# Performance work log

Measured on AMD Instinct MI355X. Metric: run time of the kernel, lower is better.

Reference implementation:

```python
import jax, jax.numpy as jnp
import numpy as np
from jax.scipy.special import logsumexp

TEMPERATURE = 0.1
EPS = 1e-8  # matches torch F.cosine_similarity eps


def setup_inputs() -> dict:
    key = jax.random.key(0)
    k1, k2 = jax.random.split(key)
    N, D, NUM_CLASSES = 8192, 256, 64
    embeddings = jax.random.normal(k1, (N, D), dtype=jnp.float32)
    target = jax.random.randint(k2, (N,), 0, NUM_CLASSES, dtype=jnp.int64)
    return {"embeddings": embeddings, "target": target}


def reference(embeddings, target):
    N = target.shape[0]
    # cosine similarity: normalize rows, then a single GEMM for all pairs
    norms = jnp.linalg.norm(embeddings, axis=-1, keepdims=True)
    e = embeddings / jnp.maximum(norms, EPS)
    sim = (e @ e.T) / TEMPERATURE  # [N, N]

    pos = target[:, None] == target[None, :]  # [N, N] bool, incl. diagonal
    diag = jnp.eye(N, dtype=bool)
    neg_inf = jnp.asarray(-jnp.inf, dtype=sim.dtype)

    # denominator: negatives only (positives masked to -inf)
    lse_neg = logsumexp(jnp.where(pos, neg_inf, sim), axis=1)
    # numerator: positives excluding self (diagonal masked to -inf)
    lse_pos = logsumexp(jnp.where(pos & ~diag, sim, neg_inf), axis=1)

    loss = lse_neg - lse_pos
    return loss.sum()
```

## Files before the change

kernel.cpp:

```cpp
#include <hip/hip_runtime.h>
#include <hip/hip_bf16.h>
#include <stdint.h>
#include <math.h>

#define NROWS 8192
#define DIM   256
#define RB    256
#define BI    128
#define JSUB  64
#define NBJS  8
#define JBLK  (JSUB*NBJS)
#define NG    (NROWS/JBLK)
#define NIT   (NROWS/BI)
#define NCLS  64
#define CAP   256

typedef __attribute__((ext_vector_type(4)))  int   int4v;
typedef __attribute__((ext_vector_type(8)))  int   int8v;
typedef __attribute__((ext_vector_type(16))) float floatx16;

typedef const __attribute__((address_space(1))) uint32_t gas_u32;
typedef __attribute__((address_space(3))) uint32_t las_u32;

#define SCALE_1_16 0x7B7B7B7B
#define L2E10      14.4269504088896f
#define CA_SCALE   (L2E10 * 16.0f)
#define CB_SCALE   16.0f

#if __has_builtin(__builtin_amdgcn_exp2f)
#define EXP2(x) __builtin_amdgcn_exp2f(x)
#else
#define EXP2(x) exp2f(x)
#endif

__device__ __forceinline__ void gload_lds16(const void* g, void* l) {
    __builtin_amdgcn_global_load_lds((gas_u32*)(uintptr_t)g,
                                     (las_u32*)(uintptr_t)l, 16, 0, 0);
}

__global__ __launch_bounds__(256) void normalize_kernel(const float* __restrict__ emb,
                                                        uint32_t* __restrict__ a8,
                                                        uint32_t* __restrict__ b8,
                                                        float* __restrict__ out)
{
    if (blockIdx.x == 0 && threadIdx.x == 0) *out = 0.f;
    int row  = blockIdx.x * 4 + (threadIdx.x >> 6);
    int lane = threadIdx.x & 63;
    float4 v = ((const float4*)(emb + (size_t)row * DIM))[lane];
    float ss = v.x*v.x + v.y*v.y + v.z*v.z + v.w*v.w;
    #pragma unroll
    for (int off = 32; off > 0; off >>= 1)
        ss += __shfl_xor(ss, off, 64);
    float inv = 1.0f / fmaxf(sqrtf(ss), 1e-8f);
    float ia = CA_SCALE * inv, ib = CB_SCALE * inv;
    int ra = __builtin_amdgcn_cvt_pk_fp8_f32(v.x * ia, v.y * ia, 0, false);
    ra     = __builtin_amdgcn_cvt_pk_fp8_f32(v.z * ia, v.w * ia, ra, true);
    int rb = __builtin_amdgcn_cvt_pk_fp8_f32(v.x * ib, v.y * ib, 0, false);
    rb     = __builtin_amdgcn_cvt_pk_fp8_f32(v.z * ib, v.w * ib, rb, true);
    a8[(size_t)row * 64 + lane] = (uint32_t)ra;
    b8[(size_t)row * 64 + lane] = (uint32_t)rb;
}

template<bool DIAG>
__device__ __forceinline__ void epi(const floatx16 acc[2],
                                    int jbs, int h, int ic0, float& ts)
{
    #pragma unroll
    for (int jt = 0; jt < 2; ++jt)
        #pragma unroll
        for (int rq = 0; rq < 4; ++rq)
            #pragma unroll
            for (int r2 = 0; r2 < 4; ++r2) {
                float v = EXP2(acc[jt][rq * 4 + r2]);
                if (DIAG) {
                    const int jg_ = jbs + jt * 32 + rq * 8 + h * 4 + r2;
                    if (jg_ == ic0) v = 0.f;
                }
                ts += v;
            }
}

__global__ __launch_bounds__(256, 4) void fused_kernel(const uint8_t* __restrict__ eA,
                                                       const uint8_t* __restrict__ eB,
                                                       const int* __restrict__ tgt,
                                                       float* __restrict__ pts,
                                                       float* __restrict__ sp)
{
    __shared__ uint8_t smem[2 * JSUB * RB];

    const int tid  = threadIdx.x;
    const int wave = tid >> 6;
    const int lane = tid & 63;
    const int col  = lane & 31;
    const int h    = lane >> 5;

    if (blockIdx.x < NCLS) {
        int* idx = (int*)smem;
        int* cnt = (int*)(smem + CAP * 4);
        const int c = blockIdx.x;
        if (tid == 0) *cnt = 0;
        __syncthreads();
        int4v tv[8];
        #pragma unroll
        for (int k = 0; k < 8; ++k)
            tv[k] = *(const int4v*)(tgt + k * 1024 + tid * 4);
        #pragma unroll
        for (int k = 0; k < 8; ++k)
            #pragma unroll
            for (int r = 0; r < 4; ++r)
                if (tv[k][r] == c) {
                    int p = atomicAdd(cnt, 1);
                    if (p < CAP) idx[p] = k * 1024 + tid * 4 + r;
                }
        __syncthreads();
        const int M   = min(*cnt, CAP);
        const int Mp  = (M + 31) & ~31;
        const int nbt = Mp >> 5;

        for (int bt = wave; bt < nbt; bt += 4) {
            const int b = bt * 32 + col;
            const uint8_t* pb = eB + (size_t)idx[min(b, M - 1)] * RB + h * 32;
            int8v bfr[4];
            #pragma unroll
            for (int s = 0; s < 4; ++s)
                bfr[s] = *(const int8v*)(pb + s * 64);
            float psum = 0.f;
            for (int at = 0; at < nbt; ++at) {
                const uint8_t* pa = eA + (size_t)idx[min(at * 32 + col, M - 1)] * RB + h * 32;
                floatx16 acc = (floatx16){0.f,0.f,0.f,0.f,0.f,0.f,0.f,0.f,
                                          0.f,0.f,0.f,0.f,0.f,0.f,0.f,0.f};
                #pragma unroll
                for (int s = 0; s < 4; ++s) {
                    int8v af = *(const int8v*)(pa + s * 64);
                    acc = __builtin_amdgcn_mfma_scale_f32_32x32x64_f8f6f4(
                        af, bfr[s], acc, 0, 0, 0, SCALE_1_16, 0, SCALE_1_16);
                }
                #pragma unroll
                for (int rq = 0; rq < 4; ++rq)
                    #pragma unroll
                    for (int r2 = 0; r2 < 4; ++r2) {
                        const int a = at * 32 + rq * 8 + h * 4 + r2;
                        float v = EXP2(acc[rq * 4 + r2]);
                        psum += (a != b && a < M) ? v : 0.f;
                    }
            }
            psum += __shfl_xor(psum, 32, 64);
            if (h == 0 && b < M) sp[idx[b]] = psum;
        }
        return;
    }

    const int g  = blockIdx.x - NCLS;
    const int bi = g & (NIT - 1);
    const int jg = g >> 6;

    const uint8_t* pb = eB + (size_t)(bi * BI + wave * 32 + col) * RB + h * 32;
    int8v bfr[4];
    #pragma unroll
    for (int s = 0; s < 4; ++s)
        bfr[s] = *(const int8v*)(pb + s * 64);

    int goffA[4];
    #pragma unroll
    for (int t = 0; t < 4; ++t) {
        int s   = wave * 256 + t * 64 + lane;
        int row = s >> 4;
        int lc  = (s & 15) ^ (row & 15);
        goffA[t] = row * RB + lc * 16;
    }
    const char* gA = (const char*)(eA + (size_t)jg * JBLK * RB);

    #pragma unroll
    for (int t = 0; t < 4; ++t)
        gload_lds16(gA + goffA[t], smem + wave * 4096 + t * 1024);

    const int ic0 = bi * BI + wave * 32 + col;

    const int xm = col & 15;
    int poff[4];
    #pragma unroll
    for (int s = 0; s < 4; ++s)
        poff[s] = ((s * 4 + h * 2) ^ xm) << 4;

    __syncthreads();

    float ts = 0.f;
    const int dpair = bi - jg * 4;

    #pragma unroll
    for (int bjs = 0; bjs < NBJS; ++bjs) {
        if (bjs < NBJS - 1) {
            const char* gAn = gA + (size_t)(bjs + 1) * JSUB * RB;
            #pragma unroll
            for (int t = 0; t < 4; ++t)
                gload_lds16(gAn + goffA[t],
                            smem + ((bjs + 1) & 1) * (JSUB * RB) + wave * 4096 + t * 1024);
        }

        const uint8_t* ab = smem + (bjs & 1) * (JSUB * RB);
        floatx16 acc[2];
        #pragma unroll
        for (int jt = 0; jt < 2; ++jt)
            acc[jt] = (floatx16){0.f,0.f,0.f,0.f,0.f,0.f,0.f,0.f,
                                 0.f,0.f,0.f,0.f,0.f,0.f,0.f,0.f};

        #pragma unroll
        for (int s = 0; s < 4; ++s) {
            int8v af[2];
            #pragma unroll
            for (int jt = 0; jt < 2; ++jt) {
                const uint8_t* pa = ab + (size_t)(jt * 32 + col) * RB;
                int4v lo = *(const int4v*)(pa + poff[s]);
                int4v hi = *(const int4v*)(pa + (poff[s] ^ 16));
                af[jt] = __builtin_shufflevector(lo, hi, 0, 1, 2, 3, 4, 5, 6, 7);
            }
            #pragma unroll
            for (int jt = 0; jt < 2; ++jt)
                acc[jt] = __builtin_amdgcn_mfma_scale_f32_32x32x64_f8f6f4(
                    af[jt], bfr[s], acc[jt], 0, 0,
                    0, SCALE_1_16, 0, SCALE_1_16);
        }

        const int jbs = jg * JBLK + bjs * JSUB;
        if ((bjs >> 1) == dpair)
            epi<true >(acc, jbs, h, ic0, ts);
        else
            epi<false>(acc, jbs, h, ic0, ts);

        if (bjs < NBJS - 1)
            __syncthreads();
    }

    ts += __shfl_xor(ts, 32, 64);
    if (h == 0)
        pts[(size_t)jg * NROWS + ic0] = ts;
}

__global__ __launch_bounds__(256) void finalize_kernel(const float* __restrict__ pts,
                                                       const float* __restrict__ sp,
                                                       float* __restrict__ out)
{
    const int i = blockIdx.x * 256 + threadIdx.x;
    float st = 0.f;
    #pragma unroll
    for (int t = 0; t < NG; ++t)
        st += pts[(size_t)t * NROWS + i];
    const float spv = sp[i];
    const float ns  = st - spv;
    float loss = logf(ns) - logf(spv);
    #pragma unroll
    for (int off = 32; off > 0; off >>= 1)
        loss += __shfl_xor(loss, off, 64);
    __shared__ float w4[4];
    if ((threadIdx.x & 63) == 0) w4[threadIdx.x >> 6] = loss;
    __syncthreads();
    if (threadIdx.x == 0)
        atomicAdd(out, w4[0] + w4[1] + w4[2] + w4[3]);
}

extern "C" void kernel_launch(void* const* d_in, const int* in_sizes, int n_in,
                              void* d_out, int out_size, void* d_ws, size_t ws_size,
                              hipStream_t stream)
{
    (void)in_sizes; (void)n_in; (void)out_size; (void)ws_size;
    const float* emb = (const float*)d_in[0];
    const int*   tgt = (const int*)d_in[1];
    float*       out = (float*)d_out;

    uint32_t* a8  = (uint32_t*)d_ws;
    uint32_t* b8  = a8 + (size_t)NROWS * 64;
    float*    pts = (float*)(b8 + (size_t)NROWS * 64);
    float*    sp  = pts + (size_t)NG * NROWS;

    normalize_kernel<<<NROWS / 4, 256, 0, stream>>>(emb, a8, b8, out);

    fused_kernel<<<NCLS + NIT * NG, 256, 0, stream>>>(
        (const uint8_t*)a8, (const uint8_t*)b8, tgt, pts, sp);

    finalize_kernel<<<NROWS / 256, 256, 0, stream>>>(pts, sp, out);
}
```

Measured before the change: 83.40 us.

## Double per-wave B-row tile so each LDS A fragment feeds four MFMAs

Doubles the row block from 128 to 256, so each wave now keeps B fragments for 64 rows in registers and issues four MFMAs per A fragment read from shared memory instead of two. This halves the number of grid blocks and the number of times each A tile is staged through LDS, which cuts global and LDS traffic per FLOP. In exchange, register use roughly doubles, launch bounds drop to 2 blocks per SM, and occupancy and latency hiding fall. The diagonal-masking block index and output indexing are adjusted to match.

```diff
diff --git a/kernel.cpp b/kernel.cpp
--- a/kernel.cpp
+++ b/kernel.cpp
@@ -6,7 +6,7 @@
 #define NROWS 8192
 #define DIM   256
 #define RB    256
-#define BI    128
+#define BI    256
 #define JSUB  64
 #define NBJS  8
 #define JBLK  (JSUB*NBJS)
@@ -62,25 +62,22 @@
 }
 
 template<bool DIAG>
-__device__ __forceinline__ void epi(const floatx16 acc[2],
-                                    int jbs, int h, int ic0, float& ts)
-{
-    #pragma unroll
-    for (int jt = 0; jt < 2; ++jt)
-        #pragma unroll
-        for (int rq = 0; rq < 4; ++rq)
-            #pragma unroll
-            for (int r2 = 0; r2 < 4; ++r2) {
-                float v = EXP2(acc[jt][rq * 4 + r2]);
-                if (DIAG) {
-                    const int jg_ = jbs + jt * 32 + rq * 8 + h * 4 + r2;
-                    if (jg_ == ic0) v = 0.f;
-                }
-                ts += v;
+__device__ __forceinline__ void epi1(const floatx16& a, int jbase, int h, int ic, float& ts)
+{
+    #pragma unroll
+    for (int rq = 0; rq < 4; ++rq)
+        #pragma unroll
+        for (int r2 = 0; r2 < 4; ++r2) {
+            float v = EXP2(a[rq * 4 + r2]);
+            if (DIAG) {
+                const int jg_ = jbase + rq * 8 + h * 4 + r2;
+                if (jg_ == ic) v = 0.f;
             }
-}
-
-__global__ __launch_bounds__(256, 4) void fused_kernel(const uint8_t* __restrict__ eA,
+            ts += v;
+        }
+}
+
+__global__ __launch_bounds__(256, 2) void fused_kernel(const uint8_t* __restrict__ eA,
                                                        const uint8_t* __restrict__ eB,
                                                        const int* __restrict__ tgt,
                                                        float* __restrict__ pts,
@@ -152,13 +149,17 @@
 
     const int g  = blockIdx.x - NCLS;
     const int bi = g & (NIT - 1);
-    const int jg = g >> 6;
-
-    const uint8_t* pb = eB + (size_t)(bi * BI + wave * 32 + col) * RB + h * 32;
-    int8v bfr[4];
-    #pragma unroll
-    for (int s = 0; s < 4; ++s)
-        bfr[s] = *(const int8v*)(pb + s * 64);
+    const int jg = g >> 5;
+
+    const uint8_t* pb0 = eB + (size_t)(bi * BI + wave * 64 + col) * RB + h * 32;
+    int8v bfr[2][4];
+    #pragma unroll
+    for (int ib = 0; ib < 2; ++ib) {
+        const uint8_t* pb = pb0 + (size_t)(ib * 32) * RB;
+        #pragma unroll
+        for (int s = 0; s < 4; ++s)
+            bfr[ib][s] = *(const int8v*)(pb + s * 64);
+    }
 
     int goffA[4];
     #pragma unroll
@@ -174,7 +175,7 @@
     for (int t = 0; t < 4; ++t)
         gload_lds16(gA + goffA[t], smem + wave * 4096 + t * 1024);
 
-    const int ic0 = bi * BI + wave * 32 + col;
+    const int ic0 = bi * BI + wave * 64 + col;
 
     const int xm = col & 15;
     int poff[4];
@@ -184,8 +185,8 @@
 
     __syncthreads();
 
-    float ts = 0.f;
-    const int dpair = bi - jg * 4;
+    float ts[2] = {0.f, 0.f};
+    const int dquad = bi - 2 * jg;
 
     #pragma unroll
     for (int bjs = 0; bjs < NBJS; ++bjs) {
@@ -198,11 +199,13 @@
         }
 
         const uint8_t* ab = smem + (bjs & 1) * (JSUB * RB);
-        floatx16 acc[2];
-        #pragma unroll
-        for (int jt = 0; jt < 2; ++jt)
-            acc[jt] = (floatx16){0.f,0.f,0.f,0.f,0.f,0.f,0.f,0.f,
-                                 0.f,0.f,0.f,0.f,0.f,0.f,0.f,0.f};
+        floatx16 acc[2][2];
+        #pragma unroll
+        for (int ib = 0; ib < 2; ++ib)
+            #pragma unroll
+            for (int jt = 0; jt < 2; ++jt)
+                acc[ib][jt] = (floatx16){0.f,0.f,0.f,0.f,0.f,0.f,0.f,0.f,
+                                         0.f,0.f,0.f,0.f,0.f,0.f,0.f,0.f};
 
         #pragma unroll
         for (int s = 0; s < 4; ++s) {
@@ -215,25 +218,39 @@
                 af[jt] = __builtin_shufflevector(lo, hi, 0, 1, 2, 3, 4, 5, 6, 7);
             }
             #pragma unroll
-            for (int jt = 0; jt < 2; ++jt)
-                acc[jt] = __builtin_amdgcn_mfma_scale_f32_32x32x64_f8f6f4(
-                    af[jt], bfr[s], acc[jt], 0, 0,
-                    0, SCALE_1_16, 0, SCALE_1_16);
+            for (int ib = 0; ib < 2; ++ib)
+                #pragma unroll
+                for (int jt = 0; jt < 2; ++jt)
+                    acc[ib][jt] = __builtin_amdgcn_mfma_scale_f32_32x32x64_f8f6f4(
+                        af[jt], bfr[ib][s], acc[ib][jt], 0, 0,
+                        0, SCALE_1_16, 0, SCALE_1_16);
         }
 
         const int jbs = jg * JBLK + bjs * JSUB;
-        if ((bjs >> 1) == dpair)
-            epi<true >(acc, jbs, h, ic0, ts);
-        else
-            epi<false>(acc, jbs, h, ic0, ts);
+        if ((bjs >> 2) == dquad) {
+            #pragma unroll
+            for (int ib = 0; ib < 2; ++ib)
+                #pragma unroll
+                for (int jt = 0; jt < 2; ++jt)
+                    epi1<true >(acc[ib][jt], jbs + jt * 32, h, ic0 + ib * 32, ts[ib]);
+        } else {
+            #pragma unroll
+            for (int ib = 0; ib < 2; ++ib)
+                #pragma unroll
+                for (int jt = 0; jt < 2; ++jt)
+                    epi1<false>(acc[ib][jt], jbs + jt * 32, h, ic0 + ib * 32, ts[ib]);
+        }
 
         if (bjs < NBJS - 1)
             __syncthreads();
     }
 
-    ts += __shfl_xor(ts, 32, 64);
-    if (h == 0)
-        pts[(size_t)jg * NROWS + ic0] = ts;
+    #pragma unroll
+    for (int ib = 0; ib < 2; ++ib) {
+        ts[ib] += __shfl_xor(ts[ib], 32, 64);
+        if (h == 0)
+            pts[(size_t)jg * NROWS + ic0 + ib * 32] = ts[ib];
+    }
 }
 
 __global__ __launch_bounds__(256) void finalize_kernel(const float* __restrict__ pts,
```

Result: slower. 87.53 us (+5.0%).

## Fuse finalize reduction into fused kernel via atomic ticket last-blocks

Applied to the files above, without the earlier changes.

Removes the separate finalize kernel launch. Each block of the fused kernel takes an atomic ticket when it finishes, and the last 32 blocks spin until every block has finished, then do the per-row log and sum reduction. This saves one launch and its gap, at the cost of a global counter, memory fences and spin-waiting in the tail blocks. Ticket order guarantees the waiting blocks are the last ones, so the spin-wait should not deadlock.

```diff
diff --git a/kernel.cpp b/kernel.cpp
--- a/kernel.cpp
+++ b/kernel.cpp
@@ -14,6 +14,8 @@
 #define NIT   (NROWS/BI)
 #define NCLS  64
 #define CAP   256
+#define TBLK  (NCLS + NIT*NG)
+#define NFIN  32
 
 typedef __attribute__((ext_vector_type(4)))  int   int4v;
 typedef __attribute__((ext_vector_type(8)))  int   int8v;
@@ -41,9 +43,10 @@
 __global__ __launch_bounds__(256) void normalize_kernel(const float* __restrict__ emb,
                                                         uint32_t* __restrict__ a8,
                                                         uint32_t* __restrict__ b8,
-                                                        float* __restrict__ out)
-{
-    if (blockIdx.x == 0 && threadIdx.x == 0) *out = 0.f;
+                                                        float* __restrict__ out,
+                                                        int* __restrict__ cc)
+{
+    if (blockIdx.x == 0 && threadIdx.x == 0) { *out = 0.f; *cc = 0; }
     int row  = blockIdx.x * 4 + (threadIdx.x >> 6);
     int lane = threadIdx.x & 63;
     float4 v = ((const float4*)(emb + (size_t)row * DIM))[lane];
@@ -84,9 +87,13 @@
                                                        const uint8_t* __restrict__ eB,
                                                        const int* __restrict__ tgt,
                                                        float* __restrict__ pts,
-                                                       float* __restrict__ sp)
+                                                       float* __restrict__ sp,
+                                                       int* __restrict__ cc,
+                                                       float* __restrict__ out)
 {
     __shared__ uint8_t smem[2 * JSUB * RB];
+    __shared__ int   ticket_s;
+    __shared__ float w4[4];
 
     const int tid  = threadIdx.x;
     const int wave = tid >> 6;
@@ -147,100 +154,106 @@
             psum += __shfl_xor(psum, 32, 64);
             if (h == 0 && b < M) sp[idx[b]] = psum;
         }
-        return;
+    } else {
+        const int g  = blockIdx.x - NCLS;
+        const int bi = g & (NIT - 1);
+        const int jg = g >> 6;
+
+        const uint8_t* pb = eB + (size_t)(bi * BI + wave * 32 + col) * RB + h * 32;
+        int8v bfr[4];
+        #pragma unroll
+        for (int s = 0; s < 4; ++s)
+            bfr[s] = *(const int8v*)(pb + s * 64);
+
+        int goffA[4];
+        #pragma unroll
+        for (int t = 0; t < 4; ++t) {
+            int s   = wave * 256 + t * 64 + lane;
+            int row = s >> 4;
+            int lc  = (s & 15) ^ (row & 15);
+            goffA[t] = row * RB + lc * 16;
+        }
+        const char* gA = (const char*)(eA + (size_t)jg * JBLK * RB);
+
+        #pragma unroll
+        for (int t = 0; t < 4; ++t)
+            gload_lds16(gA + goffA[t], smem + wave * 4096 + t * 1024);
+
+        const int ic0 = bi * BI + wave * 32 + col;
+
+        const int xm = col & 15;
+        int poff[4];
+        #pragma unroll
+        for (int s = 0; s < 4; ++s)
+            poff[s] = ((s * 4 + h * 2) ^ xm) << 4;
+
+        __syncthreads();
+
+        float ts = 0.f;
+        const int dpair = bi - jg * 4;
+
+        #pragma unroll
+        for (int bjs = 0; bjs < NBJS; ++bjs) {
+            if (bjs < NBJS - 1) {
+                const char* gAn = gA + (size_t)(bjs + 1) * JSUB * RB;
+                #pragma unroll
+                for (int t = 0; t < 4; ++t)
+                    gload_lds16(gAn + goffA[t],
+                                smem + ((bjs + 1) & 1) * (JSUB * RB) + wave * 4096 + t * 1024);
+            }
+
+            const uint8_t* ab = smem + (bjs & 1) * (JSUB * RB);
+            floatx16 acc[2];
+            #pragma unroll
+            for (int jt = 0; jt < 2; ++jt)
+                acc[jt] = (floatx16){0.f,0.f,0.f,0.f,0.f,0.f,0.f,0.f,
+                                     0.f,0.f,0.f,0.f,0.f,0.f,0.f,0.f};
+
+            #pragma unroll
+            for (int s = 0; s < 4; ++s) {
+                int8v af[2];
+                #pragma unroll
+                for (int jt = 0; jt < 2; ++jt) {
+                    const uint8_t* pa = ab + (size_t)(jt * 32 + col) * RB;
+                    int4v lo = *(const int4v*)(pa + poff[s]);
+                    int4v hi = *(const int4v*)(pa + (poff[s] ^ 16));
+                    af[jt] = __builtin_shufflevector(lo, hi, 0, 1, 2, 3, 4, 5, 6, 7);
+                }
+                #pragma unroll
+                for (int jt = 0; jt < 2; ++jt)
+                    acc[jt] = __builtin_amdgcn_mfma_scale_f32_32x32x64_f8f6f4(
+                        af[jt], bfr[s], acc[jt], 0, 0,
+                        0, SCALE_1_16, 0, SCALE_1_16);
+            }
+
+            const int jbs = jg * JBLK + bjs * JSUB;
+            if ((bjs >> 1) == dpair)
+                epi<true >(acc, jbs, h, ic0, ts);
+            else
+                epi<false>(acc, jbs, h, ic0, ts);
+
+            if (bjs < NBJS - 1)
+                __syncthreads();
+        }
+
+        ts += __shfl_xor(ts, 32, 64);
+        if (h == 0)
+            pts[(size_t)jg * NROWS + ic0] = ts;
     }
 
-    const int g  = blockIdx.x - NCLS;
-    const int bi = g & (NIT - 1);
-    const int jg = g >> 6;
-
-    const uint8_t* pb = eB + (size_t)(bi * BI + wave * 32 + col) * RB + h * 32;
-    int8v bfr[4];
-    #pragma unroll
-    for (int s = 0; s < 4; ++s)
-        bfr[s] = *(const int8v*)(pb + s * 64);
-
-    int goffA[4];
-    #pragma unroll
-    for (int t = 0; t < 4; ++t) {
-        int s   = wave * 256 + t * 64 + lane;
-        int row = s >> 4;
-        int lc  = (s & 15) ^ (row & 15);
-        goffA[t] = row * RB + lc * 16;
-    }
-    const char* gA = (const char*)(eA + (size_t)jg * JBLK * RB);
-
-    #pragma unroll
-    for (int t = 0; t < 4; ++t)
-        gload_lds16(gA + goffA[t], smem + wave * 4096 + t * 1024);
-
-    const int ic0 = bi * BI + wave * 32 + col;
-
-    const int xm = col & 15;
-    int poff[4];
-    #pragma unroll
-    for (int s = 0; s < 4; ++s)
-        poff[s] = ((s * 4 + h * 2) ^ xm) << 4;
-
-    __syncthreads();
-
-    float ts = 0.f;
-    const int dpair = bi - jg * 4;
-
-    #pragma unroll
-    for (int bjs = 0; bjs < NBJS; ++bjs) {
-        if (bjs < NBJS - 1) {
-            const char* gAn = gA + (size_t)(bjs + 1) * JSUB * RB;
-            #pragma unroll
-            for (int t = 0; t < 4; ++t)
-                gload_lds16(gAn + goffA[t],
-                            smem + ((bjs + 1) & 1) * (JSUB * RB) + wave * 4096 + t * 1024);
-        }
-
-        const uint8_t* ab = smem + (bjs & 1) * (JSUB * RB);
-        floatx16 acc[2];
-        #pragma unroll
-        for (int jt = 0; jt < 2; ++jt)
-            acc[jt] = (floatx16){0.f,0.f,0.f,0.f,0.f,0.f,0.f,0.f,
-                                 0.f,0.f,0.f,0.f,0.f,0.f,0.f,0.f};
-
-        #pragma unroll
-        for (int s = 0; s < 4; ++s) {
-            int8v af[2];
-            #pragma unroll
-            for (int jt = 0; jt < 2; ++jt) {
-                const uint8_t* pa = ab + (size_t)(jt * 32 + col) * RB;
-                int4v lo = *(const int4v*)(pa + poff[s]);
-                int4v hi = *(const int4v*)(pa + (poff[s] ^ 16));
-                af[jt] = __builtin_shufflevector(lo, hi, 0, 1, 2, 3, 4, 5, 6, 7);
-            }
-            #pragma unroll
-            for (int jt = 0; jt < 2; ++jt)
-                acc[jt] = __builtin_amdgcn_mfma_scale_f32_32x32x64_f8f6f4(
-                    af[jt], bfr[s], acc[jt], 0, 0,
-                    0, SCALE_1_16, 0, SCALE_1_16);
-        }
-
-        const int jbs = jg * JBLK + bjs * JSUB;
-        if ((bjs >> 1) == dpair)
-            epi<true >(acc, jbs, h, ic0, ts);
-        else
-            epi<false>(acc, jbs, h, ic0, ts);
-
-        if (bjs < NBJS - 1)
-            __syncthreads();
-    }
-
-    ts += __shfl_xor(ts, 32, 64);
-    if (h == 0)
-        pts[(size_t)jg * NROWS + ic0] = ts;
-}
-
-__global__ __launch_bounds__(256) void finalize_kernel(const float* __restrict__ pts,
-                                                       const float* __restrict__ sp,
-                                                       float* __restrict__ out)
-{
-    const int i = blockIdx.x * 256 + threadIdx.x;
+    __threadfence();
+    __syncthreads();
+    if (tid == 0) ticket_s = atomicAdd(cc, 1);
+    __syncthreads();
+    const int ticket = ticket_s;
+    if (ticket < TBLK - NFIN) return;
+
+    if (tid == 0)
+        while (atomicAdd(cc, 0) < TBLK) {}
+    __syncthreads();
+    __threadfence();
+
+    const int i = (ticket - (TBLK - NFIN)) * 256 + tid;
     float st = 0.f;
     #pragma unroll
     for (int t = 0; t < NG; ++t)
@@ -251,10 +264,9 @@
     #pragma unroll
     for (int off = 32; off > 0; off >>= 1)
         loss += __shfl_xor(loss, off, 64);
-    __shared__ float w4[4];
-    if ((threadIdx.x & 63) == 0) w4[threadIdx.x >> 6] = loss;
-    __syncthreads();
-    if (threadIdx.x == 0)
+    if (lane == 0) w4[wave] = loss;
+    __syncthreads();
+    if (tid == 0)
         atomicAdd(out, w4[0] + w4[1] + w4[2] + w4[3]);
 }
 
@@ -271,11 +283,10 @@
     uint32_t* b8  = a8 + (size_t)NROWS * 64;
     float*    pts = (float*)(b8 + (size_t)NROWS * 64);
     float*    sp  = pts + (size_t)NG * NROWS;
-
-    normalize_kernel<<<NROWS / 4, 256, 0, stream>>>(emb, a8, b8, out);
-
-    fused_kernel<<<NCLS + NIT * NG, 256, 0, stream>>>(
-        (const uint8_t*)a8, (const uint8_t*)b8, tgt, pts, sp);
-
-    finalize_kernel<<<NROWS / 256, 256, 0, stream>>>(pts, sp, out);
-}
+    int*      cc  = (int*)(sp + NROWS);
+
+    normalize_kernel<<<NROWS / 4, 256, 0, stream>>>(emb, a8, b8, out, cc);
+
+    fused_kernel<<<TBLK, 256, 0, stream>>>(
+        (const uint8_t*)a8, (const uint8_t*)b8, tgt, pts, sp, cc, out);
+}
```

New measurement: 169.2 us. 2.03x slower.

## Store single fp8 matrix in MFMA-fragment layout and load operands directly from global

Applied to the files above, without the earlier changes.

Replaces the two separately scaled fp8 copies (A scaled by log2e/T·16, B by 16) with one copy scaled by sqrt of the product, so the Gram-matrix scale is split symmetrically. The copy is written in a tiled layout where each 32-row block's MFMA fragments are contiguous. The fused kernel then reads A fragments straight from global/L2 with 32-byte vector loads, dropping the LDS double-buffer, the swizzled async global-to-LDS copies and the per-step barriers. This halves the normalize output and removes sync overhead. The cost is that every wave refetches A tiles from cache with no LDS reuse, and the symmetric scaling changes fp8 quantisation error.

```diff
diff --git a/kernel.cpp b/kernel.cpp
--- a/kernel.cpp
+++ b/kernel.cpp
@@ -5,7 +5,6 @@
 
 #define NROWS 8192
 #define DIM   256
-#define RB    256
 #define BI    128
 #define JSUB  64
 #define NBJS  8
@@ -19,13 +18,9 @@
 typedef __attribute__((ext_vector_type(8)))  int   int8v;
 typedef __attribute__((ext_vector_type(16))) float floatx16;
 
-typedef const __attribute__((address_space(1))) uint32_t gas_u32;
-typedef __attribute__((address_space(3))) uint32_t las_u32;
-
 #define SCALE_1_16 0x7B7B7B7B
 #define L2E10      14.4269504088896f
-#define CA_SCALE   (L2E10 * 16.0f)
-#define CB_SCALE   16.0f
+#define CE         60.772499831f
 
 #if __has_builtin(__builtin_amdgcn_exp2f)
 #define EXP2(x) __builtin_amdgcn_exp2f(x)
@@ -33,14 +28,9 @@
 #define EXP2(x) exp2f(x)
 #endif
 
-__device__ __forceinline__ void gload_lds16(const void* g, void* l) {
-    __builtin_amdgcn_global_load_lds((gas_u32*)(uintptr_t)g,
-                                     (las_u32*)(uintptr_t)l, 16, 0, 0);
-}
 
 __global__ __launch_bounds__(256) void normalize_kernel(const float* __restrict__ emb,
-                                                        uint32_t* __restrict__ a8,
-                                                        uint32_t* __restrict__ b8,
+                                                        uint32_t* __restrict__ e8,
                                                         float* __restrict__ out)
 {
     if (blockIdx.x == 0 && threadIdx.x == 0) *out = 0.f;
@@ -51,14 +41,11 @@
     #pragma unroll
     for (int off = 32; off > 0; off >>= 1)
         ss += __shfl_xor(ss, off, 64);
-    float inv = 1.0f / fmaxf(sqrtf(ss), 1e-8f);
-    float ia = CA_SCALE * inv, ib = CB_SCALE * inv;
-    int ra = __builtin_amdgcn_cvt_pk_fp8_f32(v.x * ia, v.y * ia, 0, false);
-    ra     = __builtin_amdgcn_cvt_pk_fp8_f32(v.z * ia, v.w * ia, ra, true);
-    int rb = __builtin_amdgcn_cvt_pk_fp8_f32(v.x * ib, v.y * ib, 0, false);
-    rb     = __builtin_amdgcn_cvt_pk_fp8_f32(v.z * ib, v.w * ib, rb, true);
-    a8[(size_t)row * 64 + lane] = (uint32_t)ra;
-    b8[(size_t)row * 64 + lane] = (uint32_t)rb;
+    float inv = CE / fmaxf(sqrtf(ss), 1e-8f);
+    int rw = __builtin_amdgcn_cvt_pk_fp8_f32(v.x * inv, v.y * inv, 0, false);
+    rw     = __builtin_amdgcn_cvt_pk_fp8_f32(v.z * inv, v.w * inv, rw, true);
+    e8[((size_t)(row >> 5) * 8 + (lane >> 3)) * 256 + (row & 31) * 8 + (lane & 7)] =
+        (uint32_t)rw;
 }
 
 template<bool DIAG>
@@ -80,13 +67,13 @@
             }
 }
 
-__global__ __launch_bounds__(256, 4) void fused_kernel(const uint8_t* __restrict__ eA,
-                                                       const uint8_t* __restrict__ eB,
+__global__ __launch_bounds__(256, 4) void fused_kernel(const uint8_t* __restrict__ E,
                                                        const int* __restrict__ tgt,
                                                        float* __restrict__ pts,
                                                        float* __restrict__ sp)
 {
-    __shared__ uint8_t smem[2 * JSUB * RB];
+    __shared__ int idx[CAP];
+    __shared__ int cnt;
 
     const int tid  = threadIdx.x;
     const int wave = tid >> 6;
@@ -95,10 +82,8 @@
     const int h    = lane >> 5;
 
     if (blockIdx.x < NCLS) {
-        int* idx = (int*)smem;
-        int* cnt = (int*)(smem + CAP * 4);
         const int c = blockIdx.x;
-        if (tid == 0) *cnt = 0;
+        if (tid == 0) cnt = 0;
         __syncthreads();
         int4v tv[8];
         #pragma unroll
@@ -109,29 +94,31 @@
             #pragma unroll
             for (int r = 0; r < 4; ++r)
                 if (tv[k][r] == c) {
-                    int p = atomicAdd(cnt, 1);
+                    int p = atomicAdd(&cnt, 1);
                     if (p < CAP) idx[p] = k * 1024 + tid * 4 + r;
                 }
         __syncthreads();
-        const int M   = min(*cnt, CAP);
+        const int M   = min(cnt, CAP);
         const int Mp  = (M + 31) & ~31;
         const int nbt = Mp >> 5;
 
         for (int bt = wave; bt < nbt; bt += 4) {
-            const int b = bt * 32 + col;
-            const uint8_t* pb = eB + (size_t)idx[min(b, M - 1)] * RB + h * 32;
+            const int b  = bt * 32 + col;
+            const int rb = idx[min(b, M - 1)];
+            const uint8_t* pb = E + (size_t)(rb >> 5) * 8192 + (rb & 31) * 32 + h * 1024;
             int8v bfr[4];
             #pragma unroll
             for (int s = 0; s < 4; ++s)
-                bfr[s] = *(const int8v*)(pb + s * 64);
+                bfr[s] = *(const int8v*)(pb + s * 2048);
             float psum = 0.f;
             for (int at = 0; at < nbt; ++at) {
-                const uint8_t* pa = eA + (size_t)idx[min(at * 32 + col, M - 1)] * RB + h * 32;
+                const int ra = idx[min(at * 32 + col, M - 1)];
+                const uint8_t* pa = E + (size_t)(ra >> 5) * 8192 + (ra & 31) * 32 + h * 1024;
                 floatx16 acc = (floatx16){0.f,0.f,0.f,0.f,0.f,0.f,0.f,0.f,
                                           0.f,0.f,0.f,0.f,0.f,0.f,0.f,0.f};
                 #pragma unroll
                 for (int s = 0; s < 4; ++s) {
-                    int8v af = *(const int8v*)(pa + s * 64);
+                    int8v af = *(const int8v*)(pa + s * 2048);
                     acc = __builtin_amdgcn_mfma_scale_f32_32x32x64_f8f6f4(
                         af, bfr[s], acc, 0, 0, 0, SCALE_1_16, 0, SCALE_1_16);
                 }
@@ -154,50 +141,22 @@
     const int bi = g & (NIT - 1);
     const int jg = g >> 6;
 
-    const uint8_t* pb = eB + (size_t)(bi * BI + wave * 32 + col) * RB + h * 32;
+    const uint8_t* pB = E + (size_t)(bi * 4 + wave) * 8192 + col * 32 + h * 1024;
     int8v bfr[4];
     #pragma unroll
     for (int s = 0; s < 4; ++s)
-        bfr[s] = *(const int8v*)(pb + s * 64);
-
-    int goffA[4];
-    #pragma unroll
-    for (int t = 0; t < 4; ++t) {
-        int s   = wave * 256 + t * 64 + lane;
-        int row = s >> 4;
-        int lc  = (s & 15) ^ (row & 15);
-        goffA[t] = row * RB + lc * 16;
-    }
-    const char* gA = (const char*)(eA + (size_t)jg * JBLK * RB);
-
-    #pragma unroll
-    for (int t = 0; t < 4; ++t)
-        gload_lds16(gA + goffA[t], smem + wave * 4096 + t * 1024);
+        bfr[s] = *(const int8v*)(pB + s * 2048);
 
     const int ic0 = bi * BI + wave * 32 + col;
-
-    const int xm = col & 15;
-    int poff[4];
-    #pragma unroll
-    for (int s = 0; s < 4; ++s)
-        poff[s] = ((s * 4 + h * 2) ^ xm) << 4;
-
-    __syncthreads();
+    const uint8_t* pA0 = E + (size_t)(jg * 16) * 8192 + col * 32 + h * 1024;
 
     float ts = 0.f;
     const int dpair = bi - jg * 4;
 
     #pragma unroll
     for (int bjs = 0; bjs < NBJS; ++bjs) {
-        if (bjs < NBJS - 1) {
-            const char* gAn = gA + (size_t)(bjs + 1) * JSUB * RB;
-            #pragma unroll
-            for (int t = 0; t < 4; ++t)
-                gload_lds16(gAn + goffA[t],
-                            smem + ((bjs + 1) & 1) * (JSUB * RB) + wave * 4096 + t * 1024);
-        }
-
-        const uint8_t* ab = smem + (bjs & 1) * (JSUB * RB);
+        const uint8_t* pA = pA0 + (size_t)bjs * 16384;
+
         floatx16 acc[2];
         #pragma unroll
         for (int jt = 0; jt < 2; ++jt)
@@ -206,19 +165,13 @@
 
         #pragma unroll
         for (int s = 0; s < 4; ++s) {
-            int8v af[2];
             #pragma unroll
             for (int jt = 0; jt < 2; ++jt) {
-                const uint8_t* pa = ab + (size_t)(jt * 32 + col) * RB;
-                int4v lo = *(const int4v*)(pa + poff[s]);
-                int4v hi = *(const int4v*)(pa + (poff[s] ^ 16));
-                af[jt] = __builtin_shufflevector(lo, hi, 0, 1, 2, 3, 4, 5, 6, 7);
+                int8v af = *(const int8v*)(pA + jt * 8192 + s * 2048);
+                acc[jt] = __builtin_amdgcn_mfma_scale_f32_32x32x64_f8f6f4(
+                    af, bfr[s], acc[jt], 0, 0,
+                    0, SCALE_1_16, 0, SCALE_1_16);
             }
-            #pragma unroll
-            for (int jt = 0; jt < 2; ++jt)
-                acc[jt] = __builtin_amdgcn_mfma_scale_f32_32x32x64_f8f6f4(
-                    af[jt], bfr[s], acc[jt], 0, 0,
-                    0, SCALE_1_16, 0, SCALE_1_16);
         }
 
         const int jbs = jg * JBLK + bjs * JSUB;
@@ -226,9 +179,6 @@
             epi<true >(acc, jbs, h, ic0, ts);
         else
             epi<false>(acc, jbs, h, ic0, ts);
-
-        if (bjs < NBJS - 1)
-            __syncthreads();
     }
 
     ts += __shfl_xor(ts, 32, 64);
@@ -267,15 +217,14 @@
     const int*   tgt = (const int*)d_in[1];
     float*       out = (float*)d_out;
 
-    uint32_t* a8  = (uint32_t*)d_ws;
-    uint32_t* b8  = a8 + (size_t)NROWS * 64;
-    float*    pts = (float*)(b8 + (size_t)NROWS * 64);
+    uint32_t* e8  = (uint32_t*)d_ws;
+    float*    pts = (float*)(e8 + (size_t)NROWS * 64);
     float*    sp  = pts + (size_t)NG * NROWS;
 
-    normalize_kernel<<<NROWS / 4, 256, 0, stream>>>(emb, a8, b8, out);
+    normalize_kernel<<<NROWS / 4, 256, 0, stream>>>(emb, e8, out);
 
     fused_kernel<<<NCLS + NIT * NG, 256, 0, stream>>>(
-        (const uint8_t*)a8, (const uint8_t*)b8, tgt, pts, sp);
+        (const uint8_t*)e8, tgt, pts, sp);
 
     finalize_kernel<<<NROWS / 256, 256, 0, stream>>>(pts, sp, out);
 }
```

Result: slower. 86.81 us (+4.1%).
